# Performance work log

Hardware: AMD Instinct MI355X
Metric: run time of the kernel (lower is better)

The kernel has to match this reference:

```python
import jax, jax.numpy as jnp
import numpy as np

D = 256          # input_dim == layer_size
L = 2            # n_hidden_layers in ResLinear
B, S = 8, 4096
LR = 1e-3        # AdamW learning_rate
WD = 1e-2        # weight_decay
MAX_ALR = 0.1    # max adaptive lr
EPS = 1e-8       # AdamW eps


def _lmm(Ws, bs, x):
    # ResLinear: residual MLP blocks, hidden size D.
    # Ws: [L, D, D], bs: [L, D], x: [..., D]
    for i in range(L):
        x = x + jax.nn.silu(x @ Ws[i] + bs[i])
    return x


def setup_inputs() -> dict:
    key = jax.random.key(0)
    ks = jax.random.split(key, 9)
    scale = 0.05
    return {
        "x": jax.random.normal(ks[0], (B, S, D), dtype=jnp.float32),
        "Wk": jax.random.normal(ks[1], (D, D), dtype=jnp.float32) * scale,
        "Wq": jax.random.normal(ks[2], (D, D), dtype=jnp.float32) * scale,
        "Wv": jax.random.normal(ks[3], (D, D), dtype=jnp.float32) * scale,
        "Wlr": jax.random.normal(ks[4], (D, 1), dtype=jnp.float32) * scale,
        "blr": jnp.zeros((1,), dtype=jnp.float32),
        "Ws": jax.random.normal(ks[5], (L, D, D), dtype=jnp.float32) * scale,
        "bs": jnp.zeros((L, D), dtype=jnp.float32),
    }


def reference(x, Wk, Wq, Wv, Wlr, blr, Ws, bs):
    # Projections (LinearProjection: bias-free D->D linear)
    keys = x @ Wk          # [B, S, D]
    queries = x @ Wq       # [B, S, D]
    values = x @ Wv        # [B, S, D]
    # AdaptiveLR: sigmoid gate scaled to max_adaptive_lr, one scalar per token
    alr = (jax.nn.sigmoid(x @ Wlr + blr) * MAX_ALR).reshape(-1)  # [B*S]

    def loss_fn(params):
        Ws_, bs_ = params
        preds = _lmm(Ws_, bs_, keys).reshape(-1, D)
        tgt = values.reshape(-1, D)
        per_tok = jnp.mean((preds - tgt) ** 2, axis=-1)  # [B*S]
        return jnp.sum(per_tok * alr)

    gWs, gbs = jax.grad(loss_fn)((Ws, bs))

    # Single AdamW step from zero optimizer state (step=1):
    #   m_hat = g, v_hat = g^2  ->  p' = p*(1 - lr*wd) - lr * g / (|g| + eps)
    def adamw_step(p, g):
        return p * (1.0 - LR * WD) - LR * g / (jnp.sqrt(g * g) + EPS)

    nWs = adamw_step(Ws, gWs)
    nbs = adamw_step(bs, gbs)

    retrieved = _lmm(nWs, nbs, queries)  # [B, S, D]
    # surprises = -grads
    return retrieved, -gWs, -gbs
```

## Files before the change

### kernel.cpp

```cpp
#include <hip/hip_runtime.h>
#include <math.h>


#define NTOK 32768
#define NM ((size_t)NTOK * 256)
#define LRc 1e-3f
#define WDc 1e-2f
#define EPSc 1e-8f

typedef __attribute__((ext_vector_type(8))) short bf16x8;
typedef __attribute__((ext_vector_type(4))) float f32x4;

__device__ __forceinline__ float b2f(unsigned short u) {
    union { unsigned int i; float f; } c;
    c.i = ((unsigned int)u) << 16;
    return c.f;
}
__device__ __forceinline__ unsigned short f2b(float f) {
    union { float f; unsigned int i; } c;
    c.f = f;
    unsigned int i = c.i;
    return (unsigned short)((i + 0x7FFFu + ((i >> 16) & 1u)) >> 16);
}
__device__ __forceinline__ float sigm(float z) { return 1.f / (1.f + __expf(-z)); }
__device__ __forceinline__ float siluf(float z) { return z * sigm(z); }
__device__ __forceinline__ float dsiluf(float z) {
    float s = sigm(z);
    return s * (1.f + z * (1.f - s));
}
__device__ __forceinline__ void unpack4(uint2 u, float* f) {
    f[0] = b2f(u.x & 0xFFFF); f[1] = b2f(u.x >> 16);
    f[2] = b2f(u.y & 0xFFFF); f[3] = b2f(u.y >> 16);
}
__device__ __forceinline__ uint2 pack4(const float* f) {
    uint2 o;
    o.x = (unsigned)f2b(f[0]) | ((unsigned)f2b(f[1]) << 16);
    o.y = (unsigned)f2b(f[2]) | ((unsigned)f2b(f[3]) << 16);
    return o;
}

#define WSTR 264
#define SSTR 40

template <int EPI>
__global__ __launch_bounds__(512, 4) void wgemm_k(
    const unsigned short* __restrict__ A, const unsigned short* __restrict__ Bt,
    const float* __restrict__ bias, const unsigned short* __restrict__ Rin,
    const unsigned short* __restrict__ Zin, const unsigned short* __restrict__ Vb,
    const float* __restrict__ alr, unsigned short* __restrict__ Cb,
    float* __restrict__ Cf, unsigned short* __restrict__ Zout,
    unsigned short* __restrict__ Rout, size_t zcs) {
    __shared__ unsigned short Ws[128 * WSTR];
    __shared__ unsigned short Sc[8][16 * SSTR];
    Bt += (size_t)blockIdx.z * 65536;
    Cb += (size_t)blockIdx.z * zcs;
    const int n0 = blockIdx.x * 128, m0 = blockIdx.y * 128;
    const int tid = threadIdx.x, lane = tid & 63, wv = tid >> 6;
    const int cc = lane & 15, q = lane >> 4;

    const int t0 = m0 + wv * 16;
    const unsigned short* xp = A + (size_t)(t0 + cc) * 256 + q * 8;
    bf16x8 xf[8];
#pragma unroll
    for (int c = 0; c < 8; c++) xf[c] = *(const bf16x8*)(xp + c * 32);

#pragma unroll
    for (int it = 0; it < 8; it++) {
        int i = it * 512 + tid;
        int row = i >> 5, g8 = i & 31;
        *(uint4*)&Ws[row * WSTR + g8 * 8] =
            *(const uint4*)(Bt + (size_t)(n0 + row) * 256 + g8 * 8);
    }
    __syncthreads();

    f32x4 acc[8];
#pragma unroll
    for (int t = 0; t < 8; t++) acc[t] = (f32x4){0.f, 0.f, 0.f, 0.f};

#pragma unroll
    for (int c = 0; c < 8; c++) {
#pragma unroll
        for (int nt = 0; nt < 8; nt++) {
            bf16x8 wf = *(const bf16x8*)&Ws[(nt * 16 + cc) * WSTR + c * 32 + q * 8];
            acc[nt] = __builtin_amdgcn_mfma_f32_16x16x32_bf16(wf, xf[c],
                                                              acc[nt], 0, 0, 0);
        }
    }

    const int tok = t0 + cc;
    float lalr = 0.f;
    if (EPI == 5) lalr = alr[tok] * (2.f / 256.f);
    unsigned short* sc = &Sc[wv][0];
    const int rtok = lane >> 2, roct = (lane & 3) * 8;

#pragma unroll
    for (int pr = 0; pr < 4; pr++) {
        float o2[2][4], z2[2][4];
#pragma unroll
        for (int h = 0; h < 2; h++) {
            const int nt = pr * 2 + h;
            const int gcol = n0 + nt * 16 + q * 4;
            const size_t off = (size_t)tok * 256 + gcol;
            f32x4 c = acc[nt];
            float v[4] = {c[0], c[1], c[2], c[3]};
            if (EPI == 0) {
#pragma unroll
                for (int r = 0; r < 4; r++) o2[h][r] = v[r];
            } else if (EPI == 1) {
                float bv[4], a[4];
                *(float4*)bv = *(const float4*)(bias + gcol);
                unpack4(*(const uint2*)(A + off), a);
#pragma unroll
                for (int r = 0; r < 4; r++) {
                    float z = v[r] + bv[r];
                    z2[h][r] = z;
                    o2[h][r] = a[r] + siluf(z);
                }
            } else if (EPI == 5) {
                float bv[4], a[4], vv[4];
                *(float4*)bv = *(const float4*)(bias + gcol);
                unpack4(*(const uint2*)(A + off), a);
                unpack4(*(const uint2*)(Vb + off), vv);
#pragma unroll
                for (int r = 0; r < 4; r++) {
                    float z = v[r] + bv[r];
                    float h2 = a[r] + siluf(z);
                    float dh = lalr * (h2 - vv[r]);
                    o2[h][r] = dh * dsiluf(z);
                    z2[h][r] = dh;
                }
            } else if (EPI == 2) {
                float ri[4], zi[4];
                unpack4(*(const uint2*)(Rin + off), ri);
                unpack4(*(const uint2*)(Zin + off), zi);
#pragma unroll
                for (int r = 0; r < 4; r++)
                    o2[h][r] = (v[r] + ri[r]) * dsiluf(zi[r]);
            } else {
                float bv[4], a[4];
                *(float4*)bv = *(const float4*)(bias + gcol);
                unpack4(*(const uint2*)(A + off), a);
#pragma unroll
                for (int r = 0; r < 4; r++) o2[h][r] = a[r] + siluf(v[r] + bv[r]);
            }
            if (EPI == 4) {
                *(float4*)(Cf + off) = *(float4*)o2[h];
            }
        }
        if (EPI == 4) continue;
#pragma unroll
        for (int h = 0; h < 2; h++)
            *(uint2*)&sc[cc * SSTR + h * 16 + q * 4] = pack4(o2[h]);
        uint4 pk = *(const uint4*)&sc[rtok * SSTR + roct];
        *(uint4*)(Cb + (size_t)(t0 + rtok) * 256 + n0 + pr * 32 + roct) = pk;
        if (EPI == 1 || EPI == 5) {
#pragma unroll
            for (int h = 0; h < 2; h++)
                *(uint2*)&sc[cc * SSTR + h * 16 + q * 4] = pack4(z2[h]);
            uint4 pk2 = *(const uint4*)&sc[rtok * SSTR + roct];
            unsigned short* P2 = (EPI == 1) ? Zout : Rout;
            *(uint4*)(P2 + (size_t)(t0 + rtok) * 256 + n0 + pr * 32 + roct) = pk2;
        }
    }
}

__global__ __launch_bounds__(512, 4) void rgemm_k(
    const unsigned short* __restrict__ Kb, const unsigned short* __restrict__ h1b,
    const unsigned short* __restrict__ dz0b,
    const unsigned short* __restrict__ dz1b, float* __restrict__ pbuf) {
    __shared__ unsigned short As[128 * 64];
    __shared__ unsigned short Bs2[128 * 64];
    const int z = blockIdx.z, layer = z >> 5, zc = z & 31;
    const unsigned short* Ag = layer ? h1b : Kb;
    const unsigned short* Bg = layer ? dz1b : dz0b;
    const int t0 = zc * 1024;
    const int j0 = blockIdx.x * 128, i0 = blockIdx.y * 128;
    const int tid = threadIdx.x, lane = tid & 63, wave = tid >> 6;

    const int half = tid >> 8;
    const int t9 = tid & 255;
    const int ptq = t9 >> 4;
    const int pi = (t9 & 15) * 8;
    const unsigned short* sg = half ? Bg : Ag;
    const int nb = half ? j0 : i0;
    unsigned int* dst = (unsigned int*)(half ? Bs2 : As);
    const unsigned short* gp = sg + (size_t)(t0 + ptq * 2) * 256 + nb + pi;

    const int wr = (wave >> 2) * 64, wc = (wave & 3) * 32;
    const int fr = lane & 15, fkb = lane >> 4;

    f32x4 acc[4][2];
#pragma unroll
    for (int i = 0; i < 4; i++)
#pragma unroll
        for (int j = 0; j < 2; j++) acc[i][j] = (f32x4){0.f, 0.f, 0.f, 0.f};

    uint4 u0 = *(const uint4*)gp;
    uint4 u1 = *(const uint4*)(gp + 256);
    gp += 32 * 256;

    for (int it = 0; it < 32; it++) {
        const unsigned int* w0 = (const unsigned int*)&u0;
        const unsigned int* w1 = (const unsigned int*)&u1;
#pragma unroll
        for (int ii = 0; ii < 8; ii++) {
            unsigned int lo = (w0[ii >> 1] >> (16 * (ii & 1))) & 0xFFFFu;
            unsigned int hi = (w1[ii >> 1] >> (16 * (ii & 1))) & 0xFFFFu;
            const int col = pi + ii;
            const int s2 = ((col >> 3) ^ col) & 3;
            const int s4 = ((col >> 2) ^ (col >> 5)) & 1;
            dst[col * 32 + (ptq ^ (s2 << 2) ^ (s4 << 4))] = lo | (hi << 16);
        }
        __syncthreads();
        if (it < 31) {
            u0 = *(const uint4*)gp;
            u1 = *(const uint4*)(gp + 256);
            gp += 32 * 256;
        }
        bf16x8 af[4], bfr[2];
#pragma unroll
        for (int i = 0; i < 4; i++) {
            const int col = wr + i * 16 + fr;
            const int s2 = ((col >> 3) ^ col) & 3;
            const int s4 = ((col >> 2) ^ (col >> 5)) & 1;
            af[i] = *(const bf16x8*)&As[col * 64 + (fkb ^ s2 ^ (s4 << 2)) * 8];
        }
#pragma unroll
        for (int j = 0; j < 2; j++) {
            const int col = wc + j * 16 + fr;
            const int s2 = ((col >> 3) ^ col) & 3;
            const int s4 = ((col >> 2) ^ (col >> 5)) & 1;
            bfr[j] = *(const bf16x8*)&Bs2[col * 64 + (fkb ^ s2 ^ (s4 << 2)) * 8];
        }
#pragma unroll
        for (int i = 0; i < 4; i++)
#pragma unroll
            for (int j = 0; j < 2; j++)
                acc[i][j] = __builtin_amdgcn_mfma_f32_16x16x32_bf16(
                    af[i], bfr[j], acc[i][j], 0, 0, 0);
        __syncthreads();
    }

    float* P = pbuf + (size_t)((layer << 5) + zc) * 65536;
    const int r0 = fkb * 4;
#pragma unroll
    for (int mi = 0; mi < 4; mi++)
#pragma unroll
        for (int ni = 0; ni < 2; ni++) {
            f32x4 c = acc[mi][ni];
#pragma unroll
            for (int r = 0; r < 4; r++)
                P[(size_t)(i0 + wr + mi * 16 + r0 + r) * 256 +
                  (j0 + wc + ni * 16 + fr)] = c[r];
        }
}

__global__ __launch_bounds__(256) void gradstep_k(
    const float* __restrict__ pbuf, const float* __restrict__ Ws,
    const float* __restrict__ bs, const float* __restrict__ accB,
    unsigned short* __restrict__ nWt, float* __restrict__ nb,
    float* __restrict__ outSW, float* __restrict__ outSb) {
    const int bi = blockIdx.x;
    if (bi < 512) {
        const int idx = bi * 256 + threadIdx.x;
        const int layer = idx >> 16, rc = idx & 65535;
        const float* p = pbuf + (size_t)layer * 32 * 65536 + rc;
        float g = 0.f;
#pragma unroll 8
        for (int c = 0; c < 32; c++) g += p[(size_t)c * 65536];
        outSW[idx] = -g;
        float nw = Ws[idx] * (1.f - LRc * WDc) - LRc * g / (fabsf(g) + EPSc);
        const int l = idx >> 16, k = (idx >> 8) & 255, n = idx & 255;
        nWt[(size_t)l * 65536 + n * 256 + k] = f2b(nw);
    } else {
        for (int i = threadIdx.x; i < 512; i += 256) {
            float g = accB[i];
            outSb[i] = -g;
            nb[i] = bs[i] * (1.f - LRc * WDc) - LRc * g / (fabsf(g) + EPSc);
        }
    }
}

__global__ __launch_bounds__(256) void colsum2_k(
    const unsigned short* __restrict__ dz1, const unsigned short* __restrict__ dz0,
    float* __restrict__ gb) {
    const int bi = blockIdx.x;
    const unsigned short* dz = (bi < 256) ? dz1 : dz0;
    float* g = (bi < 256) ? gb + 256 : gb;
    const int col = threadIdx.x;
    const size_t r0 = (size_t)(bi & 255) * 128;
    float s0 = 0, s1 = 0, s2 = 0, s3 = 0;
    for (int r = 0; r < 128; r += 4) {
        s0 += b2f(dz[(r0 + r) * 256 + col]);
        s1 += b2f(dz[(r0 + r + 1) * 256 + col]);
        s2 += b2f(dz[(r0 + r + 2) * 256 + col]);
        s3 += b2f(dz[(r0 + r + 3) * 256 + col]);
    }
    atomicAdd(&g[col], s0 + s1 + s2 + s3);
}

__global__ __launch_bounds__(256) void prep_all_k(
    const float* __restrict__ x, const float* __restrict__ Wlr,
    const float* __restrict__ blr, const float* __restrict__ Wk,
    const float* __restrict__ Wq, const float* __restrict__ Wv,
    const float* __restrict__ Ws, unsigned short* __restrict__ xb,
    float* __restrict__ alr, unsigned short* __restrict__ wt,
    float* __restrict__ accB) {
    const int bi = blockIdx.x;
    if (bi < 8192) {
        const int wave = threadIdx.x >> 6, lane = threadIdx.x & 63;
        const int r = bi * 4 + wave;
        float4 w = *(const float4*)(Wlr + lane * 4);
        float4 v = *(const float4*)(x + (size_t)r * 256 + lane * 4);
        float s = v.x * w.x + v.y * w.y + v.z * w.z + v.w * w.w;
        unsigned int p0 = (unsigned int)f2b(v.x) | ((unsigned int)f2b(v.y) << 16);
        unsigned int p1 = (unsigned int)f2b(v.z) | ((unsigned int)f2b(v.w) << 16);
        *(uint2*)(xb + (size_t)r * 256 + lane * 4) = make_uint2(p0, p1);
#pragma unroll
        for (int off = 32; off; off >>= 1) s += __shfl_down(s, off);
        if (lane == 0) alr[r] = 0.1f * sigm(s + blr[0]);
    } else if (bi < 9728) {
        const int b = bi - 8192;
        const int z = b >> 8;
        const int idx = (b & 255) * 256 + threadIdx.x;
        const float* src = z == 0 ? Wk : z == 1 ? Wq : z == 2 ? Wv
                         : z == 3 ? Ws : Ws + 65536;
        unsigned short* dst = wt + (size_t)z * 65536;
        float v = src[idx];
        if (z == 5)
            dst[idx] = f2b(v);
        else
            dst[(idx & 255) * 256 + (idx >> 8)] = f2b(v);
    } else {
        accB[threadIdx.x] = 0.f;
        accB[threadIdx.x + 256] = 0.f;
    }
}

extern "C" void kernel_launch(void* const* d_in, const int* in_sizes, int n_in,
                              void* d_out, int out_size, void* d_ws,
                              size_t ws_size, hipStream_t stream) {
    const float* x = (const float*)d_in[0];
    const float* Wk = (const float*)d_in[1];
    const float* Wq = (const float*)d_in[2];
    const float* Wv = (const float*)d_in[3];
    const float* Wlr = (const float*)d_in[4];
    const float* blr = (const float*)d_in[5];
    const float* Ws = (const float*)d_in[6];
    const float* bs = (const float*)d_in[7];

    unsigned short* S = (unsigned short*)d_ws;
    unsigned short* xb = S + 0 * NM;
    unsigned short* Kb = S + 1 * NM;
    unsigned short* Qb = S + 2 * NM;
    unsigned short* Vb = S + 3 * NM;
    unsigned short* z0b = S + 4 * NM;
    unsigned short* h1b = S + 5 * NM;
    unsigned short* dz1b = S + 6 * NM;
    unsigned short* dh2b = S + 7 * NM;
    unsigned short* dz0b = S + 8 * NM;
    float* pbuf = (float*)(S + 9 * NM);
    unsigned short* r1b = xb;

    unsigned short* wt = S + 11 * NM;
    unsigned short* W0t = wt + 3 * 65536;
    unsigned short* W1t = wt + 4 * 65536;
    unsigned short* W1b = wt + 5 * 65536;
    unsigned short* nW0t = wt + 6 * 65536;
    unsigned short* nW1t = wt + 7 * 65536;
    float* ft = (float*)(wt + 8 * 65536);
    float* alr = ft;
    float* accB = ft + 32768;
    float* nb = accB + 512;

    float* out_ret = (float*)d_out;
    float* out_sW = out_ret + NM;
    float* out_sb = out_sW + 131072;

    dim3 blk5(512);
    dim3 blk(256);
    dim3 g_tall(2, 256);

    prep_all_k<<<9729, blk, 0, stream>>>(x, Wlr, blr, Wk, Wq, Wv, Ws, xb, alr,
                                         wt, accB);

    wgemm_k<0><<<dim3(2, 256, 3), blk5, 0, stream>>>(
        xb, wt, nullptr, nullptr, nullptr, nullptr, nullptr, Kb, nullptr,
        nullptr, nullptr, NM);

    wgemm_k<1><<<g_tall, blk5, 0, stream>>>(Kb, W0t, bs, nullptr, nullptr,
                                            nullptr, nullptr, h1b, nullptr,
                                            z0b, nullptr, 0);

    wgemm_k<5><<<g_tall, blk5, 0, stream>>>(h1b, W1t, bs + 256, nullptr,
                                            nullptr, Vb, alr, dz1b, nullptr,
                                            nullptr, dh2b, 0);

    wgemm_k<2><<<g_tall, blk5, 0, stream>>>(dz1b, W1b, nullptr, dh2b, z0b,
                                            nullptr, nullptr, dz0b, nullptr,
                                            nullptr, nullptr, 0);

    colsum2_k<<<512, blk, 0, stream>>>(dz1b, dz0b, accB);

    rgemm_k<<<dim3(2, 2, 64), blk5, 0, stream>>>(Kb, h1b, dz0b, dz1b, pbuf);

    gradstep_k<<<513, blk, 0, stream>>>(pbuf, Ws, bs, accB, nW0t, nb, out_sW,
                                        out_sb);

    wgemm_k<3><<<g_tall, blk5, 0, stream>>>(Qb, nW0t, nb, nullptr, nullptr,
                                            nullptr, nullptr, r1b, nullptr,
                                            nullptr, nullptr, 0);
    wgemm_k<4><<<g_tall, blk5, 0, stream>>>(r1b, nW1t, nb + 256, nullptr,
                                            nullptr, nullptr, nullptr, nullptr,
                                            out_ret, nullptr, nullptr, 0);
}
```

Baseline: 252.4 us.

## Fuse bias-gradient column sums into GEMM epilogues and reuse x tile for K/Q/V

Removes the separate colsum2_k kernel and computes the bias-gradient column sums inside the dz1/dz0 GEMM epilogues. Each block reduces across its rows with lane shuffles, accumulates in shared-memory atomics, and issues one global atomic per column. The K/Q/V projection becomes one kernel that loads each token tile of x once and loops over the three weight matrices, which saves two re-reads of x. In exchange the bias sums are taken from fp32 values before bf16 rounding, and the three projections run serially within each block with fewer blocks overall.

```diff
diff --git a/kernel.cpp b/kernel.cpp
--- a/kernel.cpp
+++ b/kernel.cpp
@@ -42,18 +42,79 @@
 #define WSTR 264
 #define SSTR 40
 
+__global__ __launch_bounds__(512, 4) void wgemm3_k(
+    const unsigned short* __restrict__ A, const unsigned short* __restrict__ wt,
+    unsigned short* __restrict__ Kb, unsigned short* __restrict__ Qb,
+    unsigned short* __restrict__ Vb) {
+    __shared__ unsigned short Ws[128 * WSTR];
+    __shared__ unsigned short Sc[8][16 * SSTR];
+    const int n0 = blockIdx.x * 128, m0 = blockIdx.y * 128;
+    const int tid = threadIdx.x, lane = tid & 63, wv = tid >> 6;
+    const int cc = lane & 15, q = lane >> 4;
+    const int t0 = m0 + wv * 16;
+
+    const unsigned short* xp = A + (size_t)(t0 + cc) * 256 + q * 8;
+    bf16x8 xf[8];
+#pragma unroll
+    for (int c = 0; c < 8; c++) xf[c] = *(const bf16x8*)(xp + c * 32);
+
+    unsigned short* sc = &Sc[wv][0];
+    const int rtok = lane >> 2, roct = (lane & 3) * 8;
+    unsigned short* const outs[3] = {Kb, Qb, Vb};
+
+    for (int z = 0; z < 3; z++) {
+        __syncthreads();
+#pragma unroll
+        for (int it = 0; it < 8; it++) {
+            int i = it * 512 + tid;
+            int row = i >> 5, g8 = i & 31;
+            *(uint4*)&Ws[row * WSTR + g8 * 8] =
+                *(const uint4*)(wt + (size_t)z * 65536 +
+                                (size_t)(n0 + row) * 256 + g8 * 8);
+        }
+        __syncthreads();
+
+        f32x4 acc[8];
+#pragma unroll
+        for (int t = 0; t < 8; t++) acc[t] = (f32x4){0.f, 0.f, 0.f, 0.f};
+#pragma unroll
+        for (int c = 0; c < 8; c++) {
+#pragma unroll
+            for (int nt = 0; nt < 8; nt++) {
+                bf16x8 wf =
+                    *(const bf16x8*)&Ws[(nt * 16 + cc) * WSTR + c * 32 + q * 8];
+                acc[nt] = __builtin_amdgcn_mfma_f32_16x16x32_bf16(wf, xf[c],
+                                                                  acc[nt], 0, 0, 0);
+            }
+        }
+
+        unsigned short* Cb = outs[z];
+#pragma unroll
+        for (int pr = 0; pr < 4; pr++) {
+#pragma unroll
+            for (int h = 0; h < 2; h++) {
+                const int nt = pr * 2 + h;
+                f32x4 c = acc[nt];
+                float o[4] = {c[0], c[1], c[2], c[3]};
+                *(uint2*)&sc[cc * SSTR + h * 16 + q * 4] = pack4(o);
+            }
+            uint4 pk = *(const uint4*)&sc[rtok * SSTR + roct];
+            *(uint4*)(Cb + (size_t)(t0 + rtok) * 256 + n0 + pr * 32 + roct) = pk;
+        }
+    }
+}
+
 template <int EPI>
 __global__ __launch_bounds__(512, 4) void wgemm_k(
     const unsigned short* __restrict__ A, const unsigned short* __restrict__ Bt,
     const float* __restrict__ bias, const unsigned short* __restrict__ Rin,
     const unsigned short* __restrict__ Zin, const unsigned short* __restrict__ Vb,
-    const float* __restrict__ alr, unsigned short* __restrict__ Cb,
-    float* __restrict__ Cf, unsigned short* __restrict__ Zout,
-    unsigned short* __restrict__ Rout, size_t zcs) {
+    const float* __restrict__ alr, float* __restrict__ gB,
+    unsigned short* __restrict__ Cb, float* __restrict__ Cf,
+    unsigned short* __restrict__ Zout, unsigned short* __restrict__ Rout) {
     __shared__ unsigned short Ws[128 * WSTR];
     __shared__ unsigned short Sc[8][16 * SSTR];
-    Bt += (size_t)blockIdx.z * 65536;
-    Cb += (size_t)blockIdx.z * zcs;
+    __shared__ float accsh[128];
     const int n0 = blockIdx.x * 128, m0 = blockIdx.y * 128;
     const int tid = threadIdx.x, lane = tid & 63, wv = tid >> 6;
     const int cc = lane & 15, q = lane >> 4;
@@ -63,6 +124,10 @@
     bf16x8 xf[8];
 #pragma unroll
     for (int c = 0; c < 8; c++) xf[c] = *(const bf16x8*)(xp + c * 32);
+
+    if (EPI == 2 || EPI == 5) {
+        if (tid < 128) accsh[tid] = 0.f;
+    }
 
 #pragma unroll
     for (int it = 0; it < 8; it++) {
@@ -103,10 +168,7 @@
             const size_t off = (size_t)tok * 256 + gcol;
             f32x4 c = acc[nt];
             float v[4] = {c[0], c[1], c[2], c[3]};
-            if (EPI == 0) {
-#pragma unroll
-                for (int r = 0; r < 4; r++) o2[h][r] = v[r];
-            } else if (EPI == 1) {
+            if (EPI == 1) {
                 float bv[4], a[4];
                 *(float4*)bv = *(const float4*)(bias + gcol);
                 unpack4(*(const uint2*)(A + off), a);
@@ -146,6 +208,23 @@
             if (EPI == 4) {
                 *(float4*)(Cf + off) = *(float4*)o2[h];
             }
+            if (EPI == 2 || EPI == 5) {
+                float s0 = o2[h][0], s1 = o2[h][1], s2 = o2[h][2], s3 = o2[h][3];
+#pragma unroll
+                for (int m = 1; m < 16; m <<= 1) {
+                    s0 += __shfl_xor(s0, m);
+                    s1 += __shfl_xor(s1, m);
+                    s2 += __shfl_xor(s2, m);
+                    s3 += __shfl_xor(s3, m);
+                }
+                if (cc == 0) {
+                    const int lc = nt * 16 + q * 4;
+                    atomicAdd(&accsh[lc], s0);
+                    atomicAdd(&accsh[lc + 1], s1);
+                    atomicAdd(&accsh[lc + 2], s2);
+                    atomicAdd(&accsh[lc + 3], s3);
+                }
+            }
         }
         if (EPI == 4) continue;
 #pragma unroll
@@ -161,6 +240,10 @@
             unsigned short* P2 = (EPI == 1) ? Zout : Rout;
             *(uint4*)(P2 + (size_t)(t0 + rtok) * 256 + n0 + pr * 32 + roct) = pk2;
         }
+    }
+    if (EPI == 2 || EPI == 5) {
+        __syncthreads();
+        if (tid < 128) atomicAdd(&gB[n0 + tid], accsh[tid]);
     }
 }
 
@@ -281,24 +364,6 @@
     }
 }
 
-__global__ __launch_bounds__(256) void colsum2_k(
-    const unsigned short* __restrict__ dz1, const unsigned short* __restrict__ dz0,
-    float* __restrict__ gb) {
-    const int bi = blockIdx.x;
-    const unsigned short* dz = (bi < 256) ? dz1 : dz0;
-    float* g = (bi < 256) ? gb + 256 : gb;
-    const int col = threadIdx.x;
-    const size_t r0 = (size_t)(bi & 255) * 128;
-    float s0 = 0, s1 = 0, s2 = 0, s3 = 0;
-    for (int r = 0; r < 128; r += 4) {
-        s0 += b2f(dz[(r0 + r) * 256 + col]);
-        s1 += b2f(dz[(r0 + r + 1) * 256 + col]);
-        s2 += b2f(dz[(r0 + r + 2) * 256 + col]);
-        s3 += b2f(dz[(r0 + r + 3) * 256 + col]);
-    }
-    atomicAdd(&g[col], s0 + s1 + s2 + s3);
-}
-
 __global__ __launch_bounds__(256) void prep_all_k(
     const float* __restrict__ x, const float* __restrict__ Wlr,
     const float* __restrict__ blr, const float* __restrict__ Wk,
@@ -384,23 +449,19 @@
     prep_all_k<<<9729, blk, 0, stream>>>(x, Wlr, blr, Wk, Wq, Wv, Ws, xb, alr,
                                          wt, accB);
 
-    wgemm_k<0><<<dim3(2, 256, 3), blk5, 0, stream>>>(
-        xb, wt, nullptr, nullptr, nullptr, nullptr, nullptr, Kb, nullptr,
-        nullptr, nullptr, NM);
+    wgemm3_k<<<g_tall, blk5, 0, stream>>>(xb, wt, Kb, Qb, Vb);
 
     wgemm_k<1><<<g_tall, blk5, 0, stream>>>(Kb, W0t, bs, nullptr, nullptr,
-                                            nullptr, nullptr, h1b, nullptr,
-                                            z0b, nullptr, 0);
+                                            nullptr, nullptr, nullptr, h1b,
+                                            nullptr, z0b, nullptr);
 
     wgemm_k<5><<<g_tall, blk5, 0, stream>>>(h1b, W1t, bs + 256, nullptr,
-                                            nullptr, Vb, alr, dz1b, nullptr,
-                                            nullptr, dh2b, 0);
+                                            nullptr, Vb, alr, accB + 256,
+                                            dz1b, nullptr, nullptr, dh2b);
 
     wgemm_k<2><<<g_tall, blk5, 0, stream>>>(dz1b, W1b, nullptr, dh2b, z0b,
-                                            nullptr, nullptr, dz0b, nullptr,
-                                            nullptr, nullptr, 0);
-
-    colsum2_k<<<512, blk, 0, stream>>>(dz1b, dz0b, accB);
+                                            nullptr, nullptr, accB, dz0b,
+                                            nullptr, nullptr, nullptr);
 
     rgemm_k<<<dim3(2, 2, 64), blk5, 0, stream>>>(Kb, h1b, dz0b, dz1b, pbuf);
 
@@ -408,9 +469,9 @@
                                         out_sb);
 
     wgemm_k<3><<<g_tall, blk5, 0, stream>>>(Qb, nW0t, nb, nullptr, nullptr,
-                                            nullptr, nullptr, r1b, nullptr,
-                                            nullptr, nullptr, 0);
+                                            nullptr, nullptr, nullptr, r1b,
+                                            nullptr, nullptr, nullptr);
     wgemm_k<4><<<g_tall, blk5, 0, stream>>>(r1b, nW1t, nb + 256, nullptr,
                                             nullptr, nullptr, nullptr, nullptr,
-                                            out_ret, nullptr, nullptr, 0);
-}
+                                            nullptr, out_ret, nullptr, nullptr);
+}
```

Measured after the change: 247.3 us. 2.0% less time.

## Fuse per-layer GEMM chain into token-resident forward/backward and retrieval kernels

Applied to the files above, without the earlier changes.

Replaces the chain of separate per-layer weight GEMM launches with one fused kernel per token tile. That kernel runs layer0 forward, layer1 forward plus the loss gradient, and the layer1 backward in sequence, keeping z, h and dh packed in registers instead of writing and re-reading them through global memory. Bias-gradient column sums are folded into the epilogues through shared-memory atomics, which removes the separate colsum kernel. The retrieval path fuses both layers the same way, and the QKV projection reuses the loaded x fragments across the three weights. The price is more register pressure (launch bounds drop to 2 blocks per SM), only 256 blocks for the fused kernels, and serialized weight loads between phases.

```diff
diff --git a/kernel.cpp b/kernel.cpp
--- a/kernel.cpp
+++ b/kernel.cpp
@@ -42,126 +42,312 @@
 #define WSTR 264
 #define SSTR 40
 
-template <int EPI>
-__global__ __launch_bounds__(512, 4) void wgemm_k(
-    const unsigned short* __restrict__ A, const unsigned short* __restrict__ Bt,
-    const float* __restrict__ bias, const unsigned short* __restrict__ Rin,
-    const unsigned short* __restrict__ Zin, const unsigned short* __restrict__ Vb,
-    const float* __restrict__ alr, unsigned short* __restrict__ Cb,
-    float* __restrict__ Cf, unsigned short* __restrict__ Zout,
-    unsigned short* __restrict__ Rout, size_t zcs) {
+#define FILLW(SRC)                                                         \
+    {                                                                      \
+        _Pragma("unroll") for (int it_ = 0; it_ < 8; it_++) {              \
+            int i_ = it_ * 512 + tid;                                      \
+            int row_ = i_ >> 5, g8_ = i_ & 31;                             \
+            *(uint4*)&Ws[row_ * WSTR + g8_ * 8] =                          \
+                *(const uint4*)((SRC) + (size_t)row_ * 256 + g8_ * 8);     \
+        }                                                                  \
+    }
+
+#define MFMA_HALF(FR)                                                      \
+    {                                                                      \
+        _Pragma("unroll") for (int t_ = 0; t_ < 8; t_++) acc[t_] =         \
+            (f32x4){0.f, 0.f, 0.f, 0.f};                                   \
+        _Pragma("unroll") for (int c_ = 0; c_ < 8; c_++) {                 \
+            _Pragma("unroll") for (int nt_ = 0; nt_ < 8; nt_++) {          \
+                bf16x8 wf_ = *(const bf16x8*)&Ws[(nt_ * 16 + cc_) * WSTR + \
+                                                 c_ * 32 + q * 8];         \
+                acc[nt_] = __builtin_amdgcn_mfma_f32_16x16x32_bf16(        \
+                    wf_, (FR)[c_], acc[nt_], 0, 0, 0);                     \
+            }                                                              \
+        }                                                                  \
+    }
+
+#define COLSUM(o, base)                                                    \
+    {                                                                      \
+        float s0_ = o[0], s1_ = o[1], s2_ = o[2], s3_ = o[3];              \
+        _Pragma("unroll") for (int m_ = 1; m_ < 16; m_ <<= 1) {            \
+            s0_ += __shfl_xor(s0_, m_);                                    \
+            s1_ += __shfl_xor(s1_, m_);                                    \
+            s2_ += __shfl_xor(s2_, m_);                                    \
+            s3_ += __shfl_xor(s3_, m_);                                    \
+        }                                                                  \
+        if (cc_ == 0) {                                                    \
+            atomicAdd(&accsh[(base)], s0_);                                \
+            atomicAdd(&accsh[(base) + 1], s1_);                            \
+            atomicAdd(&accsh[(base) + 2], s2_);                            \
+            atomicAdd(&accsh[(base) + 3], s3_);                            \
+        }                                                                  \
+    }
+
+__global__ __launch_bounds__(512, 4) void wgemm3_k(
+    const unsigned short* __restrict__ A, const unsigned short* __restrict__ wt,
+    unsigned short* __restrict__ Kb, unsigned short* __restrict__ Qb,
+    unsigned short* __restrict__ Vb) {
     __shared__ unsigned short Ws[128 * WSTR];
     __shared__ unsigned short Sc[8][16 * SSTR];
-    Bt += (size_t)blockIdx.z * 65536;
-    Cb += (size_t)blockIdx.z * zcs;
     const int n0 = blockIdx.x * 128, m0 = blockIdx.y * 128;
     const int tid = threadIdx.x, lane = tid & 63, wv = tid >> 6;
-    const int cc = lane & 15, q = lane >> 4;
-
+    const int cc_ = lane & 15, q = lane >> 4;
     const int t0 = m0 + wv * 16;
-    const unsigned short* xp = A + (size_t)(t0 + cc) * 256 + q * 8;
+
+    const unsigned short* xp = A + (size_t)(t0 + cc_) * 256 + q * 8;
     bf16x8 xf[8];
 #pragma unroll
     for (int c = 0; c < 8; c++) xf[c] = *(const bf16x8*)(xp + c * 32);
 
-#pragma unroll
-    for (int it = 0; it < 8; it++) {
-        int i = it * 512 + tid;
-        int row = i >> 5, g8 = i & 31;
-        *(uint4*)&Ws[row * WSTR + g8 * 8] =
-            *(const uint4*)(Bt + (size_t)(n0 + row) * 256 + g8 * 8);
-    }
-    __syncthreads();
-
-    f32x4 acc[8];
-#pragma unroll
-    for (int t = 0; t < 8; t++) acc[t] = (f32x4){0.f, 0.f, 0.f, 0.f};
-
-#pragma unroll
-    for (int c = 0; c < 8; c++) {
-#pragma unroll
-        for (int nt = 0; nt < 8; nt++) {
-            bf16x8 wf = *(const bf16x8*)&Ws[(nt * 16 + cc) * WSTR + c * 32 + q * 8];
-            acc[nt] = __builtin_amdgcn_mfma_f32_16x16x32_bf16(wf, xf[c],
-                                                              acc[nt], 0, 0, 0);
-        }
-    }
-
-    const int tok = t0 + cc;
-    float lalr = 0.f;
-    if (EPI == 5) lalr = alr[tok] * (2.f / 256.f);
     unsigned short* sc = &Sc[wv][0];
     const int rtok = lane >> 2, roct = (lane & 3) * 8;
-
-#pragma unroll
-    for (int pr = 0; pr < 4; pr++) {
-        float o2[2][4], z2[2][4];
-#pragma unroll
-        for (int h = 0; h < 2; h++) {
-            const int nt = pr * 2 + h;
-            const int gcol = n0 + nt * 16 + q * 4;
-            const size_t off = (size_t)tok * 256 + gcol;
-            f32x4 c = acc[nt];
-            float v[4] = {c[0], c[1], c[2], c[3]};
-            if (EPI == 0) {
-#pragma unroll
-                for (int r = 0; r < 4; r++) o2[h][r] = v[r];
-            } else if (EPI == 1) {
-                float bv[4], a[4];
-                *(float4*)bv = *(const float4*)(bias + gcol);
-                unpack4(*(const uint2*)(A + off), a);
-#pragma unroll
-                for (int r = 0; r < 4; r++) {
-                    float z = v[r] + bv[r];
-                    z2[h][r] = z;
-                    o2[h][r] = a[r] + siluf(z);
-                }
-            } else if (EPI == 5) {
-                float bv[4], a[4], vv[4];
-                *(float4*)bv = *(const float4*)(bias + gcol);
-                unpack4(*(const uint2*)(A + off), a);
-                unpack4(*(const uint2*)(Vb + off), vv);
-#pragma unroll
-                for (int r = 0; r < 4; r++) {
-                    float z = v[r] + bv[r];
-                    float h2 = a[r] + siluf(z);
-                    float dh = lalr * (h2 - vv[r]);
-                    o2[h][r] = dh * dsiluf(z);
-                    z2[h][r] = dh;
-                }
-            } else if (EPI == 2) {
-                float ri[4], zi[4];
-                unpack4(*(const uint2*)(Rin + off), ri);
-                unpack4(*(const uint2*)(Zin + off), zi);
-#pragma unroll
-                for (int r = 0; r < 4; r++)
-                    o2[h][r] = (v[r] + ri[r]) * dsiluf(zi[r]);
-            } else {
-                float bv[4], a[4];
-                *(float4*)bv = *(const float4*)(bias + gcol);
-                unpack4(*(const uint2*)(A + off), a);
-#pragma unroll
-                for (int r = 0; r < 4; r++) o2[h][r] = a[r] + siluf(v[r] + bv[r]);
+    unsigned short* const outs[3] = {Kb, Qb, Vb};
+    f32x4 acc[8];
+
+    for (int z = 0; z < 3; z++) {
+        __syncthreads();
+        FILLW(wt + (size_t)z * 65536 + (size_t)n0 * 256);
+        __syncthreads();
+        MFMA_HALF(xf);
+
+        unsigned short* Cb = outs[z];
+#pragma unroll
+        for (int pr = 0; pr < 4; pr++) {
+#pragma unroll
+            for (int h = 0; h < 2; h++) {
+                const int nt = pr * 2 + h;
+                f32x4 c4 = acc[nt];
+                float o[4] = {c4[0], c4[1], c4[2], c4[3]};
+                *(uint2*)&sc[cc_ * SSTR + h * 16 + q * 4] = pack4(o);
             }
-            if (EPI == 4) {
-                *(float4*)(Cf + off) = *(float4*)o2[h];
-            }
-        }
-        if (EPI == 4) continue;
-#pragma unroll
-        for (int h = 0; h < 2; h++)
-            *(uint2*)&sc[cc * SSTR + h * 16 + q * 4] = pack4(o2[h]);
-        uint4 pk = *(const uint4*)&sc[rtok * SSTR + roct];
-        *(uint4*)(Cb + (size_t)(t0 + rtok) * 256 + n0 + pr * 32 + roct) = pk;
-        if (EPI == 1 || EPI == 5) {
-#pragma unroll
-            for (int h = 0; h < 2; h++)
-                *(uint2*)&sc[cc * SSTR + h * 16 + q * 4] = pack4(z2[h]);
-            uint4 pk2 = *(const uint4*)&sc[rtok * SSTR + roct];
-            unsigned short* P2 = (EPI == 1) ? Zout : Rout;
-            *(uint4*)(P2 + (size_t)(t0 + rtok) * 256 + n0 + pr * 32 + roct) = pk2;
-        }
-    }
+            uint4 pk = *(const uint4*)&sc[rtok * SSTR + roct];
+            *(uint4*)(Cb + (size_t)(t0 + rtok) * 256 + n0 + pr * 32 + roct) = pk;
+        }
+    }
+}
+
+__global__ __launch_bounds__(512, 2) void fwdbwd_k(
+    const unsigned short* __restrict__ Kb, const unsigned short* __restrict__ Vb,
+    const unsigned short* __restrict__ W0t, const unsigned short* __restrict__ W1t,
+    const unsigned short* __restrict__ W1bt, const float* __restrict__ bias,
+    const float* __restrict__ alr, unsigned short* __restrict__ h1b,
+    unsigned short* __restrict__ dz1b, unsigned short* __restrict__ dz0b,
+    float* __restrict__ gB) {
+    __shared__ unsigned short Ws[128 * WSTR];
+    __shared__ unsigned short Sc[8][16 * SSTR];
+    __shared__ float accsh[512];
+    const int tid = threadIdx.x, lane = tid & 63, wv = tid >> 6;
+    const int cc_ = lane & 15, q = lane >> 4;
+    const int t0 = blockIdx.x * 128 + wv * 16, tok = t0 + cc_;
+    unsigned short* sc = &Sc[wv][0];
+    const int rtok = lane >> 2, roct = (lane & 3) * 8;
+    accsh[tid] = 0.f;
+
+    const unsigned short* kp = Kb + (size_t)tok * 256 + q * 8;
+    bf16x8 kf[8];
+#pragma unroll
+    for (int c = 0; c < 8; c++) kf[c] = *(const bf16x8*)(kp + c * 32);
+    const float lalr = alr[tok] * (2.f / 256.f);
+
+    uint2 zp[16], hp[16], dp[16];
+    bf16x8 hf[8], df[8];
+    f32x4 acc[8];
+
+#define EPI_L0(H2)                                                            \
+    {                                                                         \
+        _Pragma("unroll") for (int pr = 0; pr < 4; pr++) {                    \
+            _Pragma("unroll") for (int h = 0; h < 2; h++) {                   \
+                const int nt = pr * 2 + h;                                    \
+                const int gcol = (H2) * 128 + nt * 16 + q * 4;                \
+                const size_t off = (size_t)tok * 256 + gcol;                  \
+                f32x4 c4 = acc[nt];                                           \
+                float bv[4], a[4], o[4], zz[4];                               \
+                *(float4*)bv = *(const float4*)(bias + gcol);                 \
+                unpack4(*(const uint2*)(Kb + off), a);                        \
+                _Pragma("unroll") for (int r = 0; r < 4; r++) {               \
+                    float z = c4[r] + bv[r];                                  \
+                    zz[r] = z;                                                \
+                    o[r] = a[r] + siluf(z);                                   \
+                }                                                             \
+                zp[(H2) * 8 + pr * 2 + h] = pack4(zz);                        \
+                uint2 po = pack4(o);                                          \
+                hp[(H2) * 8 + pr * 2 + h] = po;                               \
+                *(uint2*)&sc[cc_ * SSTR + h * 16 + q * 4] = po;               \
+            }                                                                 \
+            uint4 pk = *(const uint4*)&sc[rtok * SSTR + roct];                \
+            *(uint4*)(h1b + (size_t)(t0 + rtok) * 256 + (H2) * 128 +          \
+                      pr * 32 + roct) = pk;                                   \
+            hf[(H2) * 4 + pr] = *(const bf16x8*)&sc[cc_ * SSTR + q * 8];      \
+        }                                                                     \
+    }
+
+#define EPI_L1(H2)                                                            \
+    {                                                                         \
+        _Pragma("unroll") for (int pr = 0; pr < 4; pr++) {                    \
+            _Pragma("unroll") for (int h = 0; h < 2; h++) {                   \
+                const int nt = pr * 2 + h;                                    \
+                const int gcol = (H2) * 128 + nt * 16 + q * 4;                \
+                const size_t off = (size_t)tok * 256 + gcol;                  \
+                f32x4 c4 = acc[nt];                                           \
+                float bv[4], a[4], vv[4], o[4], dhv[4];                       \
+                *(float4*)bv = *(const float4*)(bias + 256 + gcol);           \
+                unpack4(hp[(H2) * 8 + pr * 2 + h], a);                        \
+                unpack4(*(const uint2*)(Vb + off), vv);                       \
+                _Pragma("unroll") for (int r = 0; r < 4; r++) {               \
+                    float z = c4[r] + bv[r];                                  \
+                    float h2v = a[r] + siluf(z);                              \
+                    float dh = lalr * (h2v - vv[r]);                          \
+                    dhv[r] = dh;                                              \
+                    o[r] = dh * dsiluf(z);                                    \
+                }                                                             \
+                dp[(H2) * 8 + pr * 2 + h] = pack4(dhv);                       \
+                *(uint2*)&sc[cc_ * SSTR + h * 16 + q * 4] = pack4(o);         \
+                COLSUM(o, 256 + gcol);                                        \
+            }                                                                 \
+            uint4 pk = *(const uint4*)&sc[rtok * SSTR + roct];                \
+            *(uint4*)(dz1b + (size_t)(t0 + rtok) * 256 + (H2) * 128 +         \
+                      pr * 32 + roct) = pk;                                   \
+            df[(H2) * 4 + pr] = *(const bf16x8*)&sc[cc_ * SSTR + q * 8];      \
+        }                                                                     \
+    }
+
+#define EPI_L2(H2)                                                            \
+    {                                                                         \
+        _Pragma("unroll") for (int pr = 0; pr < 4; pr++) {                    \
+            _Pragma("unroll") for (int h = 0; h < 2; h++) {                   \
+                const int nt = pr * 2 + h;                                    \
+                const int gcol = (H2) * 128 + nt * 16 + q * 4;                \
+                f32x4 c4 = acc[nt];                                           \
+                float ri[4], zi[4], o[4];                                     \
+                unpack4(dp[(H2) * 8 + pr * 2 + h], ri);                       \
+                unpack4(zp[(H2) * 8 + pr * 2 + h], zi);                       \
+                _Pragma("unroll") for (int r = 0; r < 4; r++) o[r] =          \
+                    (c4[r] + ri[r]) * dsiluf(zi[r]);                          \
+                *(uint2*)&sc[cc_ * SSTR + h * 16 + q * 4] = pack4(o);         \
+                COLSUM(o, gcol);                                              \
+            }                                                                 \
+            uint4 pk = *(const uint4*)&sc[rtok * SSTR + roct];                \
+            *(uint4*)(dz0b + (size_t)(t0 + rtok) * 256 + (H2) * 128 +         \
+                      pr * 32 + roct) = pk;                                   \
+        }                                                                     \
+    }
+
+    FILLW(W0t);
+    __syncthreads();
+    MFMA_HALF(kf);
+    __syncthreads();
+    FILLW(W0t + 32768);
+    EPI_L0(0);
+    __syncthreads();
+    MFMA_HALF(kf);
+    __syncthreads();
+    FILLW(W1t);
+    EPI_L0(1);
+    __syncthreads();
+    MFMA_HALF(hf);
+    __syncthreads();
+    FILLW(W1t + 32768);
+    EPI_L1(0);
+    __syncthreads();
+    MFMA_HALF(hf);
+    __syncthreads();
+    FILLW(W1bt);
+    EPI_L1(1);
+    __syncthreads();
+    MFMA_HALF(df);
+    __syncthreads();
+    FILLW(W1bt + 32768);
+    EPI_L2(0);
+    __syncthreads();
+    MFMA_HALF(df);
+    EPI_L2(1);
+    __syncthreads();
+    atomicAdd(&gB[tid], accsh[tid]);
+#undef EPI_L0
+#undef EPI_L1
+#undef EPI_L2
+}
+
+__global__ __launch_bounds__(512, 2) void ret_k(
+    const unsigned short* __restrict__ Qb, const unsigned short* __restrict__ nW0t,
+    const unsigned short* __restrict__ nW1t, const float* __restrict__ nb,
+    float* __restrict__ out_ret) {
+    __shared__ unsigned short Ws[128 * WSTR];
+    __shared__ unsigned short Sc[8][16 * SSTR];
+    const int tid = threadIdx.x, lane = tid & 63, wv = tid >> 6;
+    const int cc_ = lane & 15, q = lane >> 4;
+    const int t0 = blockIdx.x * 128 + wv * 16, tok = t0 + cc_;
+    unsigned short* sc = &Sc[wv][0];
+
+    const unsigned short* qp = Qb + (size_t)tok * 256 + q * 8;
+    bf16x8 qf[8];
+#pragma unroll
+    for (int c = 0; c < 8; c++) qf[c] = *(const bf16x8*)(qp + c * 32);
+
+    uint2 rp[16];
+    bf16x8 rf[8];
+    f32x4 acc[8];
+
+#define EPI_R0(H2)                                                            \
+    {                                                                         \
+        _Pragma("unroll") for (int pr = 0; pr < 4; pr++) {                    \
+            _Pragma("unroll") for (int h = 0; h < 2; h++) {                   \
+                const int nt = pr * 2 + h;                                    \
+                const int gcol = (H2) * 128 + nt * 16 + q * 4;                \
+                const size_t off = (size_t)tok * 256 + gcol;                  \
+                f32x4 c4 = acc[nt];                                           \
+                float bv[4], a[4], o[4];                                      \
+                *(float4*)bv = *(const float4*)(nb + gcol);                   \
+                unpack4(*(const uint2*)(Qb + off), a);                        \
+                _Pragma("unroll") for (int r = 0; r < 4; r++) o[r] =          \
+                    a[r] + siluf(c4[r] + bv[r]);                              \
+                uint2 po = pack4(o);                                          \
+                rp[(H2) * 8 + pr * 2 + h] = po;                               \
+                *(uint2*)&sc[cc_ * SSTR + h * 16 + q * 4] = po;               \
+            }                                                                 \
+            rf[(H2) * 4 + pr] = *(const bf16x8*)&sc[cc_ * SSTR + q * 8];      \
+        }                                                                     \
+    }
+
+#define EPI_R1(H2)                                                            \
+    {                                                                         \
+        _Pragma("unroll") for (int pr = 0; pr < 4; pr++) {                    \
+            _Pragma("unroll") for (int h = 0; h < 2; h++) {                   \
+                const int nt = pr * 2 + h;                                    \
+                const int gcol = (H2) * 128 + nt * 16 + q * 4;                \
+                const size_t off = (size_t)tok * 256 + gcol;                  \
+                f32x4 c4 = acc[nt];                                           \
+                float bv[4], a[4], o[4];                                      \
+                *(float4*)bv = *(const float4*)(nb + 256 + gcol);             \
+                unpack4(rp[(H2) * 8 + pr * 2 + h], a);                        \
+                _Pragma("unroll") for (int r = 0; r < 4; r++) o[r] =          \
+                    a[r] + siluf(c4[r] + bv[r]);                              \
+                *(float4*)(out_ret + off) = *(float4*)o;                      \
+            }                                                                 \
+        }                                                                     \
+    }
+
+    FILLW(nW0t);
+    __syncthreads();
+    MFMA_HALF(qf);
+    __syncthreads();
+    FILLW(nW0t + 32768);
+    EPI_R0(0);
+    __syncthreads();
+    MFMA_HALF(qf);
+    __syncthreads();
+    FILLW(nW1t);
+    EPI_R0(1);
+    __syncthreads();
+    MFMA_HALF(rf);
+    __syncthreads();
+    FILLW(nW1t + 32768);
+    EPI_R1(0);
+    __syncthreads();
+    MFMA_HALF(rf);
+    EPI_R1(1);
+#undef EPI_R0
+#undef EPI_R1
 }
 
 __global__ __launch_bounds__(512, 4) void rgemm_k(
@@ -281,24 +467,6 @@
     }
 }
 
-__global__ __launch_bounds__(256) void colsum2_k(
-    const unsigned short* __restrict__ dz1, const unsigned short* __restrict__ dz0,
-    float* __restrict__ gb) {
-    const int bi = blockIdx.x;
-    const unsigned short* dz = (bi < 256) ? dz1 : dz0;
-    float* g = (bi < 256) ? gb + 256 : gb;
-    const int col = threadIdx.x;
-    const size_t r0 = (size_t)(bi & 255) * 128;
-    float s0 = 0, s1 = 0, s2 = 0, s3 = 0;
-    for (int r = 0; r < 128; r += 4) {
-        s0 += b2f(dz[(r0 + r) * 256 + col]);
-        s1 += b2f(dz[(r0 + r + 1) * 256 + col]);
-        s2 += b2f(dz[(r0 + r + 2) * 256 + col]);
-        s3 += b2f(dz[(r0 + r + 3) * 256 + col]);
-    }
-    atomicAdd(&g[col], s0 + s1 + s2 + s3);
-}
-
 __global__ __launch_bounds__(256) void prep_all_k(
     const float* __restrict__ x, const float* __restrict__ Wlr,
     const float* __restrict__ blr, const float* __restrict__ Wk,
@@ -354,13 +522,10 @@
     unsigned short* Kb = S + 1 * NM;
     unsigned short* Qb = S + 2 * NM;
     unsigned short* Vb = S + 3 * NM;
-    unsigned short* z0b = S + 4 * NM;
     unsigned short* h1b = S + 5 * NM;
     unsigned short* dz1b = S + 6 * NM;
-    unsigned short* dh2b = S + 7 * NM;
     unsigned short* dz0b = S + 8 * NM;
     float* pbuf = (float*)(S + 9 * NM);
-    unsigned short* r1b = xb;
 
     unsigned short* wt = S + 11 * NM;
     unsigned short* W0t = wt + 3 * 65536;
@@ -379,38 +544,19 @@
 
     dim3 blk5(512);
     dim3 blk(256);
-    dim3 g_tall(2, 256);
 
     prep_all_k<<<9729, blk, 0, stream>>>(x, Wlr, blr, Wk, Wq, Wv, Ws, xb, alr,
                                          wt, accB);
 
-    wgemm_k<0><<<dim3(2, 256, 3), blk5, 0, stream>>>(
-        xb, wt, nullptr, nullptr, nullptr, nullptr, nullptr, Kb, nullptr,
-        nullptr, nullptr, NM);
-
-    wgemm_k<1><<<g_tall, blk5, 0, stream>>>(Kb, W0t, bs, nullptr, nullptr,
-                                            nullptr, nullptr, h1b, nullptr,
-                                            z0b, nullptr, 0);
-
-    wgemm_k<5><<<g_tall, blk5, 0, stream>>>(h1b, W1t, bs + 256, nullptr,
-                                            nullptr, Vb, alr, dz1b, nullptr,
-                                            nullptr, dh2b, 0);
-
-    wgemm_k<2><<<g_tall, blk5, 0, stream>>>(dz1b, W1b, nullptr, dh2b, z0b,
-                                            nullptr, nullptr, dz0b, nullptr,
-                                            nullptr, nullptr, 0);
-
-    colsum2_k<<<512, blk, 0, stream>>>(dz1b, dz0b, accB);
+    wgemm3_k<<<dim3(2, 256), blk5, 0, stream>>>(xb, wt, Kb, Qb, Vb);
+
+    fwdbwd_k<<<256, blk5, 0, stream>>>(Kb, Vb, W0t, W1t, W1b, bs, alr, h1b,
+                                       dz1b, dz0b, accB);
 
     rgemm_k<<<dim3(2, 2, 64), blk5, 0, stream>>>(Kb, h1b, dz0b, dz1b, pbuf);
 
     gradstep_k<<<513, blk, 0, stream>>>(pbuf, Ws, bs, accB, nW0t, nb, out_sW,
                                         out_sb);
 
-    wgemm_k<3><<<g_tall, blk5, 0, stream>>>(Qb, nW0t, nb, nullptr, nullptr,
-                                            nullptr, nullptr, r1b, nullptr,
-                                            nullptr, nullptr, 0);
-    wgemm_k<4><<<g_tall, blk5, 0, stream>>>(r1b, nW1t, nb + 256, nullptr,
-                                            nullptr, nullptr, nullptr, nullptr,
-                                            out_ret, nullptr, nullptr, 0);
-}
+    ret_k<<<256, blk5, 0, stream>>>(Qb, nW0t, nW1t, nb, out_ret);
+}
```

New measurement: 382.8 us. +51.6%, slower.
